# Performance work log

Measured on AMD Instinct MI355X. Metric: run time of the kernel, lower is better.

## Reference

```python
import jax, jax.numpy as jnp
import numpy as np

B, S, H, D = 4, 4096, 1024, 64

def setup_inputs() -> dict:
    key = jax.random.key(0)
    ks = jax.random.split(key, 10)
    return {
        "query": jax.random.normal(ks[0], (B, S, H), jnp.float32),
        "key": jax.random.normal(ks[1], (B, S, H), jnp.float32),
        "value": jax.random.normal(ks[2], (B, S, H), jnp.float32),
        "mask": jax.random.randint(ks[3], (B, S), 0, 2, jnp.int32),
        "Wq": jax.random.normal(ks[4], (H, D), jnp.float32) * 0.02,
        "bq": jax.random.normal(ks[5], (D,), jnp.float32) * 0.02,
        "Wk": jax.random.normal(ks[6], (H, D), jnp.float32) * 0.02,
        "bk": jax.random.normal(ks[7], (D,), jnp.float32) * 0.02,
        "Wv": jax.random.normal(ks[8], (H, D), jnp.float32) * 0.02,
        "bv": jax.random.normal(ks[9], (D,), jnp.float32) * 0.02,
    }

def reference(query, key, value, mask, Wq, bq, Wk, bk, Wv, bv):
    # single-head projections: [B,S,H] @ [H,D] -> [B,S,D]
    q = query @ Wq + bq
    k = key @ Wk + bk
    v = value @ Wv + bv
    scale = 1.0 / np.sqrt(D).astype(np.float32)
    # [B,Sq,Sk] score matrix (faithful to the unfused original)
    scores = jnp.einsum('bqd,bkd->bqk', q, k) * scale
    # mask [B,Sk] broadcast over query dim; masked positions -> -1e9
    scores = jnp.where(mask[:, None, :] == 0, jnp.float32(-1e9), scores)
    att = jax.nn.softmax(scores, axis=-1)
    # dropout prob = 0.0 -> identity
    return jnp.einsum('bqk,bkd->bqd', att, v)
```

## Files before the change

### kernel.cpp

```cpp
#include <hip/hip_runtime.h>
#include <hip/hip_bf16.h>
#include <stdint.h>


typedef __bf16 bf16;
typedef __bf16 bf16x8 __attribute__((ext_vector_type(8)));
typedef float f32x16 __attribute__((ext_vector_type(16)));

union B8 { uint4 u; bf16x8 v; uint32_t w[4]; };

#define AS1 __attribute__((address_space(1)))
#define AS3 __attribute__((address_space(3)))

__device__ __forceinline__ void async16(const void* g, void* l) {
  __builtin_amdgcn_global_load_lds((AS1 void*)(g), (AS3 void*)(l), 16, 0, 0);
}

#define KSC 0.18033688011112042f

__global__ void setup_kernel(const float* __restrict__ Wq, const float* __restrict__ Wk,
                             const float* __restrict__ Wv, const int* __restrict__ mask,
                             bf16* __restrict__ wT, float* __restrict__ biasArr)
{
  int item = blockIdx.x * 256 + threadIdx.x;
  if (item < 24576) {
    int mat = item >> 13;
    int rem = item & 8191;
    int n   = rem >> 7;
    int c   = rem & 127;
    const float* W = (mat == 0) ? Wq : (mat == 1) ? Wk : Wv;
    union { bf16 b[8]; uint4 u; } pk;
    #pragma unroll
    for (int j = 0; j < 8; ++j)
      pk.b[j] = (bf16)W[(c * 8 + j) * 64 + n];
    bf16* o = wT + mat * 65536;
    *(uint4*)(o + n * 1024 + c * 8) = pk.u;
  } else {
    int i = (item - 24576) << 2;
    const int4 m = *(const int4*)(mask + i);
    float4 b;
    b.x = m.x ? 0.0f : -1e30f;
    b.y = m.y ? 0.0f : -1e30f;
    b.z = m.z ? 0.0f : -1e30f;
    b.w = m.w ? 0.0f : -1e30f;
    *(float4*)(biasArr + i) = b;
  }
}

__global__ __launch_bounds__(128) void proj_kernel(
    const float* __restrict__ Xq, const float* __restrict__ Xk, const float* __restrict__ Xv,
    const bf16* __restrict__ wT,
    const float* __restrict__ bq, const float* __restrict__ bk, const float* __restrict__ bv,
    bf16* __restrict__ qo, bf16* __restrict__ ko, bf16* __restrict__ vTo)
{
  const int bx = blockIdx.x;
  const int mat = bx >> 9;
  const int m0 = (bx & 511) << 5;
  const float* X    = (mat == 0) ? Xq : (mat == 1) ? Xk : Xv;
  const float* bias = (mat == 0) ? bq : (mat == 1) ? bk : bv;
  const bf16* w = wT + mat * 65536;

  __shared__ __align__(16) float xbuf[2][32 * 64];
  __shared__ __align__(16) bf16 cs[32 * 64];

  const int tid  = threadIdx.x;
  const int wv   = tid >> 6;
  const int lane = tid & 63;
  const int half = lane >> 5;
  const int ln   = lane & 31;

  const int drow = lane >> 4;
  const int dcl  = lane & 15;

  const float* xb = X + (size_t)m0 * 1024;
  const bf16*  w0 = w + ((wv << 5) + ln) * 1024 + half * 8;

  float b0v = bias[(wv << 5) + ln];
  asm volatile("s_waitcnt vmcnt(0)" ::: "memory");

  #pragma unroll
  for (int i = 0; i < 4; ++i) {
    int ii = (wv << 2) + i;
    int row = ii * 4 + drow;
    int sc = (dcl & 8) | ((dcl ^ (row & 7)) & 7);
    async16(xb + (size_t)row * 1024 + sc * 4, &xbuf[0][ii * 256]);
  }
  uint4 wc[4], wn[4];
  #pragma unroll
  for (int s = 0; s < 4; ++s)
    wc[s] = *(const uint4*)(w0 + s * 16);

  f32x16 acc = {};

  for (int c = 0; c < 16; ++c) {
    if (c < 15) {
      const float* src = xb + (c + 1) * 64;
      #pragma unroll
      for (int i = 0; i < 4; ++i) {
        int ii = (wv << 2) + i;
        int row = ii * 4 + drow;
        int sc = (dcl & 8) | ((dcl ^ (row & 7)) & 7);
        async16(src + (size_t)row * 1024 + sc * 4, &xbuf[(c + 1) & 1][ii * 256]);
      }
      #pragma unroll
      for (int s = 0; s < 4; ++s)
        wn[s] = *(const uint4*)(w0 + (c + 1) * 64 + s * 16);
      asm volatile("s_waitcnt vmcnt(8)" ::: "memory");
    } else {
      asm volatile("s_waitcnt vmcnt(0)" ::: "memory");
    }
    __builtin_amdgcn_s_barrier();
    asm volatile("" ::: "memory");

    const float* xl = &xbuf[c & 1][0];
    #pragma unroll
    for (int s = 0; s < 4; ++s) {
      int lc = s * 4 + half * 2;
      int p0 = (lc & 8) | ((lc ^ (ln & 7)) & 7);
      int p1 = ((lc + 1) & 8) | (((lc + 1) ^ (ln & 7)) & 7);
      float4 fa = *(const float4*)(xl + ln * 64 + p0 * 4);
      float4 fb = *(const float4*)(xl + ln * 64 + p1 * 4);
      union { bf16 b[8]; bf16x8 v; } af;
      af.b[0] = (bf16)fa.x; af.b[1] = (bf16)fa.y;
      af.b[2] = (bf16)fa.z; af.b[3] = (bf16)fa.w;
      af.b[4] = (bf16)fb.x; af.b[5] = (bf16)fb.y;
      af.b[6] = (bf16)fb.z; af.b[7] = (bf16)fb.w;
      B8 wa; wa.u = wc[s];
      acc = __builtin_amdgcn_mfma_f32_32x32x16_bf16(af.v, wa.v, acc, 0, 0, 0);
    }
    asm volatile("s_waitcnt lgkmcnt(0)" ::: "memory");
    __builtin_amdgcn_s_barrier();
    #pragma unroll
    for (int s = 0; s < 4; ++s) wc[s] = wn[s];
  }

  #pragma unroll
  for (int r = 0; r < 16; ++r) {
    int mrow = (r & 3) + 8 * (r >> 2) + 4 * half;
    cs[mrow * 64 + (wv << 5) + ln] = (bf16)(acc[r] + b0v);
  }
  __syncthreads();

  if (mat < 2) {
    bf16* gout = (mat == 0) ? qo : ko;
    #pragma unroll
    for (int p = 0; p < 2; ++p) {
      int id = p * 128 + tid;
      int r = id >> 3;
      int c = id & 7;
      int phys = c ^ (r & 7);
      *(uint4*)(gout + (size_t)(m0 + r) * 64 + phys * 8) = *(const uint4*)(cs + r * 64 + c * 8);
    }
  } else {
    int batch = m0 >> 12;
    int sk = m0 & 4095;
    int tb = sk & ~63;
    int halfTile = (sk >> 5) & 1;
    #pragma unroll
    for (int p = 0; p < 2; ++p) {
      int id = p * 128 + tid;
      int d = id >> 2;
      int j = id & 3;
      union { bf16 b[8]; uint4 u; } pk;
      #pragma unroll
      for (int t = 0; t < 8; ++t) pk.b[t] = cs[(j * 8 + t) * 64 + d];
      int cl = halfTile * 4 + j;
      int phys = cl ^ (d & 7);
      *(uint4*)(vTo + ((size_t)batch * 64 + d) * 4096 + tb + phys * 8) = pk.u;
    }
  }
}

__global__ __launch_bounds__(256, 2) void flash_kernel(
    const bf16* __restrict__ qb, const bf16* __restrict__ kb, const bf16* __restrict__ vT,
    const float* __restrict__ biasArr, float* __restrict__ out)
{
  __shared__ __align__(16) char smem[65536];
  bf16* ksb = (bf16*)smem;
  bf16* vsb = (bf16*)(smem + 32768);

  const int tid = threadIdx.x;
  const int lane = tid & 63;
  const int wv = tid >> 6;
  const int half = lane >> 5;
  const int ln = lane & 31;

  const int batch = blockIdx.x >> 6;
  const int q0 = (blockIdx.x & 63) << 6;

  bf16x8 qf[2][4];
  const bf16* qbase = qb + ((size_t)batch * 4096 + q0) * 64;
  #pragma unroll
  for (int qk = 0; qk < 2; ++qk)
  #pragma unroll
  for (int s = 0; s < 4; ++s) {
    int qq = (qk << 5) + ln;
    int phys = (2 * s + half) ^ (qq & 7);
    B8 t; t.u = *(const uint4*)(qbase + qq * 64 + phys * 8);
    qf[qk][s] = t.v;
  }

  f32x16 acc[2][2] = {{{}, {}}, {{}, {}}};
  float den0 = 0.f, den1 = 0.f;

  bf16* kds = ksb + wv * 4096;
  bf16* vds = vsb + wv * 4096;
  const bf16* kgb = kb + (size_t)batch * 4096 * 64;
  const bf16* vgb = vT + (size_t)batch * 64 * 4096;
  const float* barr = biasArr + batch * 4096;

  for (int it = 0; it < 16; ++it) {
    const int key0 = wv * 1024 + it * 64;
    __syncthreads();
    const bf16* ksrc = kgb + (size_t)key0 * 64;
    #pragma unroll
    for (int i = 0; i < 8; ++i)
      async16((const char*)ksrc + i * 1024 + lane * 16, (char*)kds + i * 1024);
    const bf16* vsrc = vgb + key0;
    #pragma unroll
    for (int i = 0; i < 8; ++i)
      async16((const char*)vsrc + ((size_t)(i * 8 + (lane >> 3)) * 4096 + (lane & 7) * 8) * 2,
              (char*)vds + i * 1024);
    __syncthreads();

    #pragma unroll
    for (int st = 0; st < 2; ++st) {
      f32x16 s0 = {};
      f32x16 s1 = {};
      #pragma unroll
      for (int s = 0; s < 4; ++s) {
        int key = (st << 5) + ln;
        B8 af; af.u = *(const uint4*)(kds + key * 64 + (((2 * s + half) ^ (key & 7)) << 3));
        s0 = __builtin_amdgcn_mfma_f32_32x32x16_bf16(af.v, qf[0][s], s0, 0, 0, 0);
        s1 = __builtin_amdgcn_mfma_f32_32x32x16_bf16(af.v, qf[1][s], s1, 0, 0, 0);
      }
      float bb[16];
      #pragma unroll
      for (int g = 0; g < 4; ++g)
        *(float4*)&bb[4 * g] = *(const float4*)(barr + key0 + (st << 5) + 8 * g + (half << 2));
      uint32_t pk0[8], pk1[8];
      #pragma unroll
      for (int i = 0; i < 8; ++i) {
        float a0 = __builtin_amdgcn_exp2f(fmaf(s0[2 * i],     KSC, bb[2 * i]));
        float a1 = __builtin_amdgcn_exp2f(fmaf(s0[2 * i + 1], KSC, bb[2 * i + 1]));
        float c0 = __builtin_amdgcn_exp2f(fmaf(s1[2 * i],     KSC, bb[2 * i]));
        float c1 = __builtin_amdgcn_exp2f(fmaf(s1[2 * i + 1], KSC, bb[2 * i + 1]));
        den0 += a0 + a1;
        den1 += c0 + c1;
        union { bf16 b[2]; uint32_t u; } u0, u1;
        u0.b[0] = (bf16)a0; u0.b[1] = (bf16)a1;
        u1.b[0] = (bf16)c0; u1.b[1] = (bf16)c1;
        pk0[i] = u0.u; pk1[i] = u1.u;
      }
      uint32_t xp0[8], xp1[8];
      #pragma unroll
      for (int i = 0; i < 8; ++i) {
        xp0[i] = (uint32_t)__shfl_xor((int)pk0[i], 32);
        xp1[i] = (uint32_t)__shfl_xor((int)pk1[i], 32);
      }
      #pragma unroll
      for (int t = 0; t < 2; ++t) {
        B8 p0f, p1f;
        p0f.w[0] = half ? xp0[4 * t + 2] : pk0[4 * t];
        p0f.w[1] = half ? xp0[4 * t + 3] : pk0[4 * t + 1];
        p0f.w[2] = half ? pk0[4 * t + 2] : xp0[4 * t];
        p0f.w[3] = half ? pk0[4 * t + 3] : xp0[4 * t + 1];
        p1f.w[0] = half ? xp1[4 * t + 2] : pk1[4 * t];
        p1f.w[1] = half ? xp1[4 * t + 3] : pk1[4 * t + 1];
        p1f.w[2] = half ? pk1[4 * t + 2] : xp1[4 * t];
        p1f.w[3] = half ? pk1[4 * t + 3] : xp1[4 * t + 1];
        #pragma unroll
        for (int dh = 0; dh < 2; ++dh) {
          int d = (dh << 5) + ln;
          B8 vf; vf.u = *(const uint4*)(vds + d * 64 +
                          ((((st << 2) + (t << 1) + half) ^ (d & 7)) << 3));
          acc[0][dh] = __builtin_amdgcn_mfma_f32_32x32x16_bf16(vf.v, p0f.v, acc[0][dh], 0, 0, 0);
          acc[1][dh] = __builtin_amdgcn_mfma_f32_32x32x16_bf16(vf.v, p1f.v, acc[1][dh], 0, 0, 0);
        }
      }
    }
  }

  den0 += __shfl_xor(den0, 32);
  den1 += __shfl_xor(den1, 32);

  float* nb = (float*)smem;
  float* dn = (float*)(smem + 34816);

  __syncthreads();
  if (wv >= 2) {
    float* mynb = nb + (wv - 2) * 4352;
    #pragma unroll
    for (int qk = 0; qk < 2; ++qk)
    #pragma unroll
    for (int dh = 0; dh < 2; ++dh)
    #pragma unroll
    for (int g = 0; g < 4; ++g) {
      int q = (qk << 5) + ln;
      int d = 8 * g + (half << 2) + (dh << 5);
      f32x16 a = acc[qk][dh];
      *(float4*)(mynb + q * 68 + d) = make_float4(a[4*g], a[4*g+1], a[4*g+2], a[4*g+3]);
    }
    if (half == 0) {
      dn[(wv - 2) * 64 + ln]      = den0;
      dn[(wv - 2) * 64 + 32 + ln] = den1;
    }
  }
  __syncthreads();
  if (wv < 2) {
    float* pb = nb + wv * 4352;
    #pragma unroll
    for (int qk = 0; qk < 2; ++qk)
    #pragma unroll
    for (int dh = 0; dh < 2; ++dh)
    #pragma unroll
    for (int g = 0; g < 4; ++g) {
      int q = (qk << 5) + ln;
      int d = 8 * g + (half << 2) + (dh << 5);
      float4 t = *(const float4*)(pb + q * 68 + d);
      acc[qk][dh][4*g+0] += t.x; acc[qk][dh][4*g+1] += t.y;
      acc[qk][dh][4*g+2] += t.z; acc[qk][dh][4*g+3] += t.w;
    }
    den0 += dn[wv * 64 + ln];
    den1 += dn[wv * 64 + 32 + ln];
  }
  __syncthreads();
  if (wv < 2) {
    float* mynb = nb + wv * 4352;
    #pragma unroll
    for (int qk = 0; qk < 2; ++qk)
    #pragma unroll
    for (int dh = 0; dh < 2; ++dh)
    #pragma unroll
    for (int g = 0; g < 4; ++g) {
      int q = (qk << 5) + ln;
      int d = 8 * g + (half << 2) + (dh << 5);
      f32x16 a = acc[qk][dh];
      *(float4*)(mynb + q * 68 + d) = make_float4(a[4*g], a[4*g+1], a[4*g+2], a[4*g+3]);
    }
    if (half == 0) {
      dn[wv * 64 + ln]      = den0;
      dn[wv * 64 + 32 + ln] = den1;
    }
  }
  __syncthreads();
  #pragma unroll
  for (int p = 0; p < 4; ++p) {
    int i = p * 256 + tid;
    int qq = i >> 4;
    int d4 = (i & 15) << 2;
    float4 A = *(const float4*)(nb + qq * 68 + d4);
    float4 Bv = *(const float4*)(nb + 4352 + qq * 68 + d4);
    float dd = dn[qq] + dn[64 + qq];
    float inv = 1.0f / dd;
    float4 o = make_float4((A.x + Bv.x) * inv, (A.y + Bv.y) * inv,
                           (A.z + Bv.z) * inv, (A.w + Bv.w) * inv);
    *(float4*)(out + ((size_t)batch * 4096 + q0 + qq) * 64 + d4) = o;
  }
}

extern "C" void kernel_launch(void* const* d_in, const int* in_sizes, int n_in,
                              void* d_out, int out_size, void* d_ws, size_t ws_size,
                              hipStream_t stream)
{
  const float* query = (const float*)d_in[0];
  const float* key   = (const float*)d_in[1];
  const float* value = (const float*)d_in[2];
  const int*   mask  = (const int*)d_in[3];
  const float* Wq    = (const float*)d_in[4];
  const float* bq    = (const float*)d_in[5];
  const float* Wk    = (const float*)d_in[6];
  const float* bk    = (const float*)d_in[7];
  const float* Wv    = (const float*)d_in[8];
  const float* bv    = (const float*)d_in[9];
  float* out = (float*)d_out;

  bf16* qb = (bf16*)d_ws;
  bf16* kb = qb + 1048576;
  bf16* vT = kb + 1048576;
  bf16* wT = vT + 1048576;
  float* biasArr = (float*)((char*)d_ws + 3 * 2097152 + 393216);

  setup_kernel<<<112, 256, 0, stream>>>(Wq, Wk, Wv, mask, wT, biasArr);
  proj_kernel<<<1536, 128, 0, stream>>>(query, key, value, wT, bq, bk, bv, qb, kb, vT);
  flash_kernel<<<256, 256, 0, stream>>>(qb, kb, vT, biasArr, out);
}
```

Measured before the change: 264.9 us.

## Replace async LDS loads in projection with register-staged two-deep prefetch pipeline

The projection kernel stops using global_load_lds direct-to-LDS copies. Instead it loads X tiles into registers two chunks ahead, writes them to LDS after each MFMA step, and fully unrolls the 16-step K loop with one barrier per step. It also adds a minimum-occupancy hint of 3 blocks to the launch bounds. The aim is deeper latency hiding and fewer waits per iteration, at the cost of more VGPRs and a possible spill risk under the occupancy constraint.

```diff
diff --git a/kernel.cpp b/kernel.cpp
--- a/kernel.cpp
+++ b/kernel.cpp
@@ -47,7 +47,7 @@
   }
 }
 
-__global__ __launch_bounds__(128) void proj_kernel(
+__global__ __launch_bounds__(128, 3) void proj_kernel(
     const float* __restrict__ Xq, const float* __restrict__ Xk, const float* __restrict__ Xv,
     const bf16* __restrict__ wT,
     const float* __restrict__ bq, const float* __restrict__ bk, const float* __restrict__ bv,
@@ -76,41 +76,45 @@
   const bf16*  w0 = w + ((wv << 5) + ln) * 1024 + half * 8;
 
   float b0v = bias[(wv << 5) + ln];
-  asm volatile("s_waitcnt vmcnt(0)" ::: "memory");
-
-  #pragma unroll
-  for (int i = 0; i < 4; ++i) {
-    int ii = (wv << 2) + i;
-    int row = ii * 4 + drow;
-    int sc = (dcl & 8) | ((dcl ^ (row & 7)) & 7);
-    async16(xb + (size_t)row * 1024 + sc * 4, &xbuf[0][ii * 256]);
-  }
-  uint4 wc[4], wn[4];
-  #pragma unroll
-  for (int s = 0; s < 4; ++s)
-    wc[s] = *(const uint4*)(w0 + s * 16);
+
+  float4 xr[2][4];
+  uint4  wr[2][4];
+
+  #define ISSUE_X(j)                                                     \
+    { const float* src_ = xb + (j) * 64;                                 \
+      _Pragma("unroll")                                                  \
+      for (int i_ = 0; i_ < 4; ++i_) {                                   \
+        int ii_ = (wv << 2) + i_;                                        \
+        int row_ = ii_ * 4 + drow;                                       \
+        int sc_ = (dcl & 8) | ((dcl ^ (row_ & 7)) & 7);                  \
+        xr[(j) & 1][i_] = *(const float4*)(src_ + (size_t)row_ * 1024 + sc_ * 4); } }
+
+  #define ISSUE_W(j)                                                     \
+    { _Pragma("unroll")                                                  \
+      for (int s_ = 0; s_ < 4; ++s_)                                     \
+        wr[(j) & 1][s_] = *(const uint4*)(w0 + (j) * 64 + s_ * 16); }
+
+  #define WRITE_X(j)                                                     \
+    { float* d_ = &xbuf[(j) & 1][0];                                     \
+      _Pragma("unroll")                                                  \
+      for (int i_ = 0; i_ < 4; ++i_) {                                   \
+        int ii_ = (wv << 2) + i_;                                        \
+        *(float4*)(d_ + ii_ * 256 + lane * 4) = xr[(j) & 1][i_]; } }
+
+  ISSUE_X(0);
+  ISSUE_X(1);
+  ISSUE_W(0);
+  WRITE_X(0);
+  asm volatile("s_waitcnt lgkmcnt(0)" ::: "memory");
+  __builtin_amdgcn_s_barrier();
+  asm volatile("" ::: "memory");
 
   f32x16 acc = {};
 
+  #pragma unroll
   for (int c = 0; c < 16; ++c) {
-    if (c < 15) {
-      const float* src = xb + (c + 1) * 64;
-      #pragma unroll
-      for (int i = 0; i < 4; ++i) {
-        int ii = (wv << 2) + i;
-        int row = ii * 4 + drow;
-        int sc = (dcl & 8) | ((dcl ^ (row & 7)) & 7);
-        async16(src + (size_t)row * 1024 + sc * 4, &xbuf[(c + 1) & 1][ii * 256]);
-      }
-      #pragma unroll
-      for (int s = 0; s < 4; ++s)
-        wn[s] = *(const uint4*)(w0 + (c + 1) * 64 + s * 16);
-      asm volatile("s_waitcnt vmcnt(8)" ::: "memory");
-    } else {
-      asm volatile("s_waitcnt vmcnt(0)" ::: "memory");
-    }
-    __builtin_amdgcn_s_barrier();
-    asm volatile("" ::: "memory");
+    if (c < 14) ISSUE_X(c + 2);
+    if (c < 15) ISSUE_W(c + 1);
 
     const float* xl = &xbuf[c & 1][0];
     #pragma unroll
@@ -125,14 +129,21 @@
       af.b[2] = (bf16)fa.z; af.b[3] = (bf16)fa.w;
       af.b[4] = (bf16)fb.x; af.b[5] = (bf16)fb.y;
       af.b[6] = (bf16)fb.z; af.b[7] = (bf16)fb.w;
-      B8 wa; wa.u = wc[s];
+      B8 wa; wa.u = wr[c & 1][s];
       acc = __builtin_amdgcn_mfma_f32_32x32x16_bf16(af.v, wa.v, acc, 0, 0, 0);
     }
-    asm volatile("s_waitcnt lgkmcnt(0)" ::: "memory");
-    __builtin_amdgcn_s_barrier();
-    #pragma unroll
-    for (int s = 0; s < 4; ++s) wc[s] = wn[s];
-  }
+
+    if (c < 15) {
+      WRITE_X(c + 1);
+      asm volatile("s_waitcnt lgkmcnt(0)" ::: "memory");
+      __builtin_amdgcn_s_barrier();
+      asm volatile("" ::: "memory");
+    }
+  }
+
+  #undef ISSUE_X
+  #undef ISSUE_W
+  #undef WRITE_X
 
   #pragma unroll
   for (int r = 0; r < 16; ++r) {
```

Result: slower. 295.3 us (+11.5%).
